# Performance work log

Hardware: AMD Instinct MI355X
Metric: run time of the kernel (lower is better)

The kernel has to match this reference:

```python
import jax, jax.numpy as jnp
import numpy as np

B, S, HID = 8, 2048, 1024
H, DH = 16, 64
EPS = 1e-12  # torch F.normalize eps


def _heads(x):
    # [B,S,HID] -> [B,H,S,DH]
    return x.reshape(B, S, H, DH).transpose(0, 2, 1, 3)


def _l2norm(x):
    n = jnp.sqrt(jnp.sum(x * x, axis=-1, keepdims=True))
    return x / jnp.maximum(n, EPS)


def setup_inputs() -> dict:
    key = jax.random.key(0)
    ks = jax.random.split(key, 4)
    sc = 0.02
    return {
        "hidden_states": jax.random.normal(ks[0], (B, S, HID), jnp.float32),
        "attention_mask": jnp.zeros((B, 1, 1, S), jnp.int32),
        "Wq": jax.random.normal(ks[1], (HID, HID), jnp.float32) * sc,
        "bq": jnp.zeros((HID,), jnp.float32),
        "Wk": jax.random.normal(ks[2], (HID, HID), jnp.float32) * sc,
        "bk": jnp.zeros((HID,), jnp.float32),
        "Wv": jax.random.normal(ks[3], (HID, HID), jnp.float32) * sc,
        "bv": jnp.zeros((HID,), jnp.float32),
    }


def reference(hidden_states, attention_mask, Wq, bq, Wk, bk, Wv, bv):
    # QKV projections (nn.Linear: x @ W^T + b; here W stored as [in,out]-equivalent square)
    q = _heads(hidden_states @ Wq + bq)  # [B,H,S,DH]
    k = _heads(hidden_states @ Wk + bk)
    v = _heads(hidden_states @ Wv + bv)

    # mask == 0 -> valid token; transpose(-1,-2): [B,1,1,S] -> [B,1,S,1]
    mask = (attention_mask == 0).astype(q.dtype)            # [B,1,1,S]
    mask_t = jnp.swapaxes(mask, -1, -2)                      # [B,1,S,1]
    q = q * mask_t
    k = k * mask_t
    v = v * mask_t

    q = _l2norm(q)
    k = _l2norm(k)
    v = v / mask.sum(-1)[..., None]                          # divide by valid-token count

    if q.shape[-1] > q.shape[-2]:
        # DH > S: explicit O(S^2) path
        ctx = jnp.einsum("bhsq,bhqd->bhsd", jnp.einsum("bhse,bhqe->bhsq", q, k), v)
    else:
        # linear-attention order: Q @ (K^T V), O(S*DH^2)
        kv = jnp.einsum("bhse,bhsd->bhed", k, v)             # [B,H,DH,DH]
        ctx = jnp.einsum("bhse,bhed->bhsd", q, kv)

    return ctx.transpose(0, 2, 1, 3).reshape(B, S, HID)
```

## Files before the change

### kernel.cpp

```cpp
#include <hip/hip_runtime.h>
#include <stdint.h>

#define B_    8
#define S_    2048
#define HID_  1024
#define H_    16
#define DH_   64
#define M_    (B_ * S_)

using bf16x8 = __attribute__((ext_vector_type(8))) __bf16;
using bf16x4 = __attribute__((ext_vector_type(4))) __bf16;
using f32x4  = __attribute__((ext_vector_type(4))) float;

__device__ __forceinline__ void gload_lds16(const void* g, void* l) {
  __builtin_amdgcn_global_load_lds(
      (const __attribute__((address_space(1))) void*)g,
      (__attribute__((address_space(3))) void*)l, 16, 0, 0);
}

__global__ void cast_hs(const float* __restrict__ hs, __bf16* __restrict__ out, int n8) {
  int i = blockIdx.x * blockDim.x + threadIdx.x;
  int stride = gridDim.x * blockDim.x;
  for (; i < n8; i += stride) {
    const float4* p = (const float4*)(hs + (size_t)i * 8);
    float4 a = p[0], c = p[1];
    bf16x8 v;
    v[0] = (__bf16)a.x; v[1] = (__bf16)a.y; v[2] = (__bf16)a.z; v[3] = (__bf16)a.w;
    v[4] = (__bf16)c.x; v[5] = (__bf16)c.y; v[6] = (__bf16)c.z; v[7] = (__bf16)c.w;
    *(bf16x8*)(out + (size_t)i * 8) = v;
  }
}

__global__ void transpose_w(const float* __restrict__ Wq, const float* __restrict__ Wk,
                            const float* __restrict__ Wv, __bf16* __restrict__ Wt) {
  __shared__ float tile[32][33];
  int w = blockIdx.z;
  const float* W = (w == 0) ? Wq : (w == 1) ? Wk : Wv;
  int k0 = blockIdx.x * 32, n0 = blockIdx.y * 32;
  int tx = threadIdx.x, ty = threadIdx.y;
#pragma unroll
  for (int i = 0; i < 4; ++i)
    tile[ty * 4 + i][tx] = W[(size_t)(k0 + ty * 4 + i) * HID_ + n0 + tx];
  __syncthreads();
#pragma unroll
  for (int i = 0; i < 4; ++i)
    Wt[(size_t)w * HID_ * HID_ + (size_t)(n0 + ty * 4 + i) * HID_ + k0 + tx] =
        (__bf16)tile[tx][ty * 4 + i];
}

__global__ void mask_prep(const int* __restrict__ mask, float* __restrict__ validf,
                          float* __restrict__ counts) {
  __shared__ float red[256];
  int b = blockIdx.x;
  float cnt = 0.f;
  for (int s = threadIdx.x; s < S_; s += 256) {
    float v = (mask[b * S_ + s] == 0) ? 1.f : 0.f;
    validf[b * S_ + s] = v;
    cnt += v;
  }
  red[threadIdx.x] = cnt;
  __syncthreads();
  for (int off = 128; off > 0; off >>= 1) {
    if (threadIdx.x < off) red[threadIdx.x] += red[threadIdx.x + off];
    __syncthreads();
  }
  if (threadIdx.x == 0) counts[b] = red[0];
}

__global__ __launch_bounds__(512, 2) void qkv_gemm8(
    const __bf16* __restrict__ hsb, const __bf16* __restrict__ Wt,
    const float* __restrict__ biasq, const float* __restrict__ biask,
    const float* __restrict__ biasv, const float* __restrict__ validf,
    const float* __restrict__ counts, __bf16* __restrict__ qn,
    __bf16* __restrict__ kT, __bf16* __restrict__ vT) {
  __shared__ __bf16 As[2][2][128 * 64];
  __shared__ __bf16 Bs[2][2][128 * 64];

  int bid = blockIdx.x;
  int swz = (bid & 7) * 96 + (bid >> 3);
  int tm = swz / 12;
  int tnw = swz - tm * 12;
  int tn = tnw & 3;
  int w  = tnw >> 2;

  int tid = threadIdx.x;
  int lane = tid & 63, wid = tid >> 6;
  int lr = lane & 15, g = lane >> 4;
  int wr = wid >> 2, wcn = wid & 3;

  int m0 = tm * 256, n0 = tn * 256;
  const __bf16* Bsrc = Wt + (size_t)w * (HID_ * HID_);

  int srow = tid >> 3;
  int scol = ((tid & 7) ^ (srow & 7)) << 3;
  int soff = tid * 16;

  auto stA = [&](int t_, int ah) {
    const __bf16* s0 = hsb + (size_t)(m0 + ah * 128 + srow) * HID_ + t_ * 64 + scol;
    char* d = (char*)&As[t_ & 1][ah][0] + soff;
    gload_lds16(s0, d);
    gload_lds16(s0 + (size_t)64 * HID_, d + 8192);
  };
  auto stB = [&](int t_, int bh) {
    const __bf16* s0 = Bsrc + (size_t)(n0 + bh * 128 + srow) * HID_ + t_ * 64 + scol;
    char* d = (char*)&Bs[t_ & 1][bh][0] + soff;
    gload_lds16(s0, d);
    gload_lds16(s0 + (size_t)64 * HID_, d + 8192);
  };

  int swz8 = (lr & 7) << 4;
  int arow = wr * 64 + lr;
  int brow = (wcn & 1) * 64 + lr;
  int bsel = wcn >> 1;

  f32x4 acc[8][4] = {};

#define PHASE(MH, KK, STAGE, VM)                                              \
  {                                                                           \
    bf16x8 fa[4], fb[4];                                                      \
    const char* abase = (const char*)&As[buf][MH][0];                         \
    const char* bbase = (const char*)&Bs[buf][bsel][0];                       \
    _Pragma("unroll")                                                         \
    for (int mf = 0; mf < 4; ++mf)                                            \
      fa[mf] = *(const bf16x8*)(abase + (arow + mf * 16) * 128 +              \
                                (((KK) * 64 + g * 16) ^ swz8));               \
    _Pragma("unroll")                                                         \
    for (int nf = 0; nf < 4; ++nf)                                            \
      fb[nf] = *(const bf16x8*)(bbase + (brow + nf * 16) * 128 +              \
                                (((KK) * 64 + g * 16) ^ swz8));               \
    STAGE;                                                                    \
    VM;                                                                       \
    __builtin_amdgcn_s_barrier();                                             \
    asm volatile("s_waitcnt lgkmcnt(0)" ::: "memory");                        \
    __builtin_amdgcn_sched_barrier(0);                                        \
    __builtin_amdgcn_s_setprio(1);                                            \
    _Pragma("unroll")                                                         \
    for (int mf = 0; mf < 4; ++mf)                                            \
      _Pragma("unroll")                                                       \
      for (int nf = 0; nf < 4; ++nf)                                          \
        acc[(MH) * 4 + mf][nf] = __builtin_amdgcn_mfma_f32_16x16x32_bf16(     \
            fa[mf], fb[nf], acc[(MH) * 4 + mf][nf], 0, 0, 0);                 \
    __builtin_amdgcn_s_setprio(0);                                            \
    __builtin_amdgcn_s_barrier();                                             \
  }

  stA(0, 0); stA(0, 1); stB(0, 0); stB(0, 1); stA(1, 0);
  asm volatile("s_waitcnt vmcnt(2)" ::: "memory");
  __builtin_amdgcn_s_barrier();

  for (int t = 0; t < 16; ++t) {
    int buf = t & 1;
    PHASE(0, 0, { if (t < 15) stA(t + 1, 1); }, {});
    PHASE(0, 1, { if (t < 15) stB(t + 1, 0); }, {});
    PHASE(1, 0, { if (t < 15) stB(t + 1, 1); }, {});
    PHASE(1, 1, { if (t < 14) stA(t + 2, 0); },
          {
            if (t < 14)       asm volatile("s_waitcnt vmcnt(2)" ::: "memory");
            else if (t == 14) asm volatile("s_waitcnt vmcnt(0)" ::: "memory");
          });
  }
#undef PHASE

  const float* bias = (w == 0) ? biasq : (w == 1) ? biask : biasv;
  float bb[4];
#pragma unroll
  for (int nf = 0; nf < 4; ++nf) bb[nf] = bias[n0 + wcn * 64 + nf * 16 + lr];

  int batch = m0 >> 11;
  float invcnt = 1.0f / counts[batch];
  int h = tn * 4 + wcn;

#pragma unroll
  for (int m = 0; m < 8; ++m) {
    int mh = m >> 2, mf = m & 3;
    int rbase = m0 + mh * 128 + wr * 64 + mf * 16 + g * 4;
    float vld[4];
#pragma unroll
    for (int j = 0; j < 4; ++j) vld[j] = validf[rbase + j];
    float ss[4] = {0.f, 0.f, 0.f, 0.f};
#pragma unroll
    for (int nf = 0; nf < 4; ++nf)
#pragma unroll
      for (int j = 0; j < 4; ++j) {
        float x = (acc[m][nf][j] + bb[nf]) * vld[j];
        acc[m][nf][j] = x;
        ss[j] += x * x;
      }
    float sc[4];
#pragma unroll
    for (int j = 0; j < 4; ++j) {
      float s = ss[j];
      s += __shfl_xor(s, 1);
      s += __shfl_xor(s, 2);
      s += __shfl_xor(s, 4);
      s += __shfl_xor(s, 8);
      if (w == 2) sc[j] = vld[j] * invcnt;
      else        sc[j] = 1.0f / fmaxf(sqrtf(s), 1e-12f);
    }
    if (w == 0) {
#pragma unroll
      for (int nf = 0; nf < 4; ++nf) {
        int c = n0 + wcn * 64 + nf * 16 + lr;
#pragma unroll
        for (int j = 0; j < 4; ++j)
          qn[(size_t)(rbase + j) * HID_ + c] = (__bf16)(acc[m][nf][j] * sc[j]);
      }
    } else {
      __bf16* dst = (w == 1) ? kT : vT;
      int sbase = rbase & (S_ - 1);
#pragma unroll
      for (int nf = 0; nf < 4; ++nf) {
        int d = nf * 16 + lr;
        bf16x4 pk;
#pragma unroll
        for (int j = 0; j < 4; ++j) pk[j] = (__bf16)(acc[m][nf][j] * sc[j]);
        *(bf16x4*)(dst + (size_t)((batch * H_ + h) * DH_ + d) * S_ + sbase) = pk;
      }
    }
  }
}

__global__ __launch_bounds__(256) void kv_gemm(const __bf16* __restrict__ kT,
                                               const __bf16* __restrict__ vT,
                                               __bf16* __restrict__ vk) {
  __shared__ __align__(16) char smem[65536];
  __bf16* kbuf = (__bf16*)smem;
  __bf16* vbuf = (__bf16*)(smem + 32768);

  int bh = blockIdx.x;
  int tid = threadIdx.x, lane = tid & 63, wid = tid >> 6;
  int g = lane >> 4, lr = lane & 15;
  const __bf16* kb = kT + (size_t)bh * DH_ * S_;
  const __bf16* vb = vT + (size_t)bh * DH_ * S_;

  f32x4 acc[4][4] = {};

  for (int sc0 = 0; sc0 < S_; sc0 += 256) {
#pragma unroll
    for (int it = 0; it < 8; ++it) {
      int seg = tid + it * 256;
      int row = seg >> 5, col = (seg & 31) * 8;
      gload_lds16(kb + (size_t)row * S_ + sc0 + col, (void*)(kbuf + seg * 8));
      gload_lds16(vb + (size_t)row * S_ + sc0 + col, (void*)(vbuf + seg * 8));
    }
    __syncthreads();
    int sl = wid * 64;
#pragma unroll
    for (int kk = 0; kk < 64; kk += 32) {
      bf16x8 fa[4], fb[4];
#pragma unroll
      for (int m = 0; m < 4; ++m)
        fa[m] = *(const bf16x8*)(vbuf + (m * 16 + lr) * 256 + sl + kk + g * 8);
#pragma unroll
      for (int n = 0; n < 4; ++n)
        fb[n] = *(const bf16x8*)(kbuf + (n * 16 + lr) * 256 + sl + kk + g * 8);
#pragma unroll
      for (int m = 0; m < 4; ++m)
#pragma unroll
        for (int n = 0; n < 4; ++n)
          acc[m][n] = __builtin_amdgcn_mfma_f32_16x16x32_bf16(fa[m], fb[n], acc[m][n], 0, 0, 0);
    }
    __syncthreads();
  }

  float* red = (float*)smem;
#pragma unroll
  for (int m = 0; m < 4; ++m)
#pragma unroll
    for (int n = 0; n < 4; ++n)
#pragma unroll
      for (int j = 0; j < 4; ++j)
        red[wid * 4096 + (m * 16 + g * 4 + j) * 64 + n * 16 + lr] = acc[m][n][j];
  __syncthreads();
  for (int idx = tid; idx < 4096; idx += 256) {
    float s = red[idx] + red[4096 + idx] + red[8192 + idx] + red[12288 + idx];
    vk[(size_t)bh * 4096 + idx] = (__bf16)s;
  }
}

__global__ __launch_bounds__(256) void ctx_gemm(const __bf16* __restrict__ qn,
                                                const __bf16* __restrict__ vk,
                                                float* __restrict__ out) {
  __shared__ __align__(16) __bf16 qbuf[128 * 64];
  __shared__ __align__(16) __bf16 wbuf[64 * 64];

  int st = blockIdx.x;
  int bh = blockIdx.y;
  int b = bh >> 4, h = bh & 15;
  int tid = threadIdx.x, lane = tid & 63, wid = tid >> 6;
  int g = lane >> 4, lr = lane & 15;
  int s0 = st * 128;

#pragma unroll
  for (int it = 0; it < 4; ++it) {
    int seg = tid + it * 256;
    int row = seg >> 3, col = (seg & 7) * 8;
    gload_lds16(qn + (size_t)(b * S_ + s0 + row) * HID_ + h * DH_ + col,
                (void*)(qbuf + seg * 8));
  }
#pragma unroll
  for (int it = 0; it < 2; ++it) {
    int seg = tid + it * 256;
    gload_lds16(vk + (size_t)bh * 4096 + seg * 8, (void*)(wbuf + seg * 8));
  }
  __syncthreads();

  f32x4 acc[2][4] = {};
#pragma unroll
  for (int kk = 0; kk < 64; kk += 32) {
    bf16x8 fa[2], fb[4];
#pragma unroll
    for (int m = 0; m < 2; ++m)
      fa[m] = *(const bf16x8*)(qbuf + (wid * 32 + m * 16 + lr) * 64 + kk + g * 8);
#pragma unroll
    for (int n = 0; n < 4; ++n)
      fb[n] = *(const bf16x8*)(wbuf + (n * 16 + lr) * 64 + kk + g * 8);
#pragma unroll
    for (int m = 0; m < 2; ++m)
#pragma unroll
      for (int n = 0; n < 4; ++n)
        acc[m][n] = __builtin_amdgcn_mfma_f32_16x16x32_bf16(fa[m], fb[n], acc[m][n], 0, 0, 0);
  }

#pragma unroll
  for (int m = 0; m < 2; ++m) {
    int rbase = s0 + wid * 32 + m * 16 + g * 4;
#pragma unroll
    for (int n = 0; n < 4; ++n) {
      int d = n * 16 + lr;
#pragma unroll
      for (int j = 0; j < 4; ++j)
        out[(size_t)(b * S_ + rbase + j) * HID_ + h * DH_ + d] = acc[m][n][j];
    }
  }
}

extern "C" void kernel_launch(void* const* d_in, const int* in_sizes, int n_in,
                              void* d_out, int out_size, void* d_ws, size_t ws_size,
                              hipStream_t stream) {
  const float* hs   = (const float*)d_in[0];
  const int*   mask = (const int*)d_in[1];
  const float* Wq   = (const float*)d_in[2];
  const float* bq   = (const float*)d_in[3];
  const float* Wk   = (const float*)d_in[4];
  const float* bk   = (const float*)d_in[5];
  const float* Wv   = (const float*)d_in[6];
  const float* bv   = (const float*)d_in[7];
  float* out = (float*)d_out;

  char* ws = (char*)d_ws;
  __bf16* hsb    = (__bf16*)(ws);
  __bf16* Wt     = (__bf16*)(ws + (33554432));
  __bf16* qn     = (__bf16*)(ws + (41943040));
  __bf16* kT     = (__bf16*)(ws + (75497472));
  __bf16* vT     = (__bf16*)(ws + (109051904));
  __bf16* vk     = (__bf16*)(ws + (142606336));
  float*  validf = (float*)(ws + (143654912));
  float*  counts = (float*)(ws + (143654912) + 65536);

  cast_hs<<<2048, 256, 0, stream>>>(hs, hsb, (B_ * S_ * HID_) / 8);
  transpose_w<<<dim3(32, 32, 3), dim3(32, 8), 0, stream>>>(Wq, Wk, Wv, Wt);
  mask_prep<<<8, 256, 0, stream>>>(mask, validf, counts);
  qkv_gemm8<<<768, 512, 0, stream>>>(hsb, Wt, bq, bk, bv, validf, counts, qn, kT, vT);
  kv_gemm<<<128, 256, 0, stream>>>(kT, vT, vk);
  ctx_gemm<<<dim3(16, 128), 256, 0, stream>>>(qn, vk, out);
}
```

Measured before the change: 208.5 us.

## Restructure GEMM main loop to overlap LDS fragment reads with MFMA clusters

Replaces the four barrier-separated phases per K-tile with one barrier per tile. Fragment reads for the next MFMA cluster are issued ahead and gated by partial lgkmcnt waits, so LDS latency hides behind MFMA work. Global-to-LDS prefetch for the next tile is spread across the clusters, and the loop is unrolled by two. The cost is more fragment registers live at once and a full vmcnt(0) wait at the top of each tile, which may expose global load latency that the old staggered prefetch hid.

```diff
diff --git a/kernel.cpp b/kernel.cpp
--- a/kernel.cpp
+++ b/kernel.cpp
@@ -114,52 +114,68 @@
   int bsel = wcn >> 1;
 
   f32x4 acc[8][4] = {};
-
-#define PHASE(MH, KK, STAGE, VM)                                              \
-  {                                                                           \
-    bf16x8 fa[4], fb[4];                                                      \
-    const char* abase = (const char*)&As[buf][MH][0];                         \
-    const char* bbase = (const char*)&Bs[buf][bsel][0];                       \
-    _Pragma("unroll")                                                         \
-    for (int mf = 0; mf < 4; ++mf)                                            \
-      fa[mf] = *(const bf16x8*)(abase + (arow + mf * 16) * 128 +              \
-                                (((KK) * 64 + g * 16) ^ swz8));               \
+  bf16x8 fb[4], fbN[4], fa0[4], fa1[4];
+
+#define RD_A(DST, BUF, MH, KK)                                                \
+  _Pragma("unroll")                                                           \
+  for (int mf = 0; mf < 4; ++mf)                                              \
+    DST[mf] = *(const bf16x8*)((const char*)&As[BUF][MH][0] +                 \
+                               (arow + mf * 16) * 128 +                       \
+                               (((KK) * 64 + g * 16) ^ swz8));                \
+  __builtin_amdgcn_sched_barrier(0);
+
+#define RD_B(DST, BUF, KK)                                                    \
+  _Pragma("unroll")                                                           \
+  for (int nf = 0; nf < 4; ++nf)                                              \
+    DST[nf] = *(const bf16x8*)((const char*)&Bs[BUF][bsel][0] +               \
+                               (brow + nf * 16) * 128 +                       \
+                               (((KK) * 64 + g * 16) ^ swz8));                \
+  __builtin_amdgcn_sched_barrier(0);
+
+#define CLUSTER(ACCB, FA, FB, LG)                                             \
+  asm volatile("s_waitcnt lgkmcnt(" #LG ")" ::: "memory");                    \
+  __builtin_amdgcn_sched_barrier(0);                                          \
+  __builtin_amdgcn_s_setprio(1);                                              \
+  _Pragma("unroll")                                                           \
+  for (int mf = 0; mf < 4; ++mf)                                              \
     _Pragma("unroll")                                                         \
     for (int nf = 0; nf < 4; ++nf)                                            \
-      fb[nf] = *(const bf16x8*)(bbase + (brow + nf * 16) * 128 +              \
-                                (((KK) * 64 + g * 16) ^ swz8));               \
-    STAGE;                                                                    \
-    VM;                                                                       \
-    __builtin_amdgcn_s_barrier();                                             \
-    asm volatile("s_waitcnt lgkmcnt(0)" ::: "memory");                        \
-    __builtin_amdgcn_sched_barrier(0);                                        \
-    __builtin_amdgcn_s_setprio(1);                                            \
-    _Pragma("unroll")                                                         \
-    for (int mf = 0; mf < 4; ++mf)                                            \
-      _Pragma("unroll")                                                       \
-      for (int nf = 0; nf < 4; ++nf)                                          \
-        acc[(MH) * 4 + mf][nf] = __builtin_amdgcn_mfma_f32_16x16x32_bf16(     \
-            fa[mf], fb[nf], acc[(MH) * 4 + mf][nf], 0, 0, 0);                 \
-    __builtin_amdgcn_s_setprio(0);                                            \
-    __builtin_amdgcn_s_barrier();                                             \
-  }
-
-  stA(0, 0); stA(0, 1); stB(0, 0); stB(0, 1); stA(1, 0);
-  asm volatile("s_waitcnt vmcnt(2)" ::: "memory");
-  __builtin_amdgcn_s_barrier();
-
+      acc[(ACCB) + mf][nf] = __builtin_amdgcn_mfma_f32_16x16x32_bf16(         \
+          FA[mf], FB[nf], acc[(ACCB) + mf][nf], 0, 0, 0);                     \
+  __builtin_amdgcn_s_setprio(0);                                              \
+  __builtin_amdgcn_sched_barrier(0);
+
+  stA(0, 0); stA(0, 1); stB(0, 0); stB(0, 1);
+
+#pragma unroll 2
   for (int t = 0; t < 16; ++t) {
     int buf = t & 1;
-    PHASE(0, 0, { if (t < 15) stA(t + 1, 1); }, {});
-    PHASE(0, 1, { if (t < 15) stB(t + 1, 0); }, {});
-    PHASE(1, 0, { if (t < 15) stB(t + 1, 1); }, {});
-    PHASE(1, 1, { if (t < 14) stA(t + 2, 0); },
-          {
-            if (t < 14)       asm volatile("s_waitcnt vmcnt(2)" ::: "memory");
-            else if (t == 14) asm volatile("s_waitcnt vmcnt(0)" ::: "memory");
-          });
-  }
-#undef PHASE
+    asm volatile("s_waitcnt vmcnt(0)" ::: "memory");
+    __builtin_amdgcn_s_barrier();
+    __builtin_amdgcn_sched_barrier(0);
+
+    RD_B(fb,  buf, 0);
+    RD_A(fa0, buf, 0, 0);
+    RD_A(fa1, buf, 1, 0);
+    if (t < 15) { stA(t + 1, 0); stA(t + 1, 1); }
+
+    CLUSTER(0, fa0, fb, 4)
+
+    RD_B(fbN, buf, 1);
+    RD_A(fa0, buf, 0, 1);
+    if (t < 15) stB(t + 1, 0);
+
+    CLUSTER(4, fa1, fb, 8)
+
+    RD_A(fa1, buf, 1, 1);
+    if (t < 15) stB(t + 1, 1);
+
+    CLUSTER(0, fa0, fbN, 4)
+    CLUSTER(4, fa1, fbN, 0)
+  }
+#undef RD_A
+#undef RD_B
+#undef CLUSTER
 
   const float* bias = (w == 0) ? biasq : (w == 1) ? biask : biasv;
   float bb[4];
```

Measured after the change: 184.9 us. -11.3%, faster.
